# Kernel optimization log

Hardware: AMD Instinct MI355X
Metric: run time of the kernel (lower is better)

Reference implementation:

```python
import jax, jax.numpy as jnp
import numpy as np

DIM = 2048; KV_RANK = 512; Q_RANK = 768; H = 16
D_NR = 128; D_R = 64; D_V = 128
B = 8; L = 32; MAX_T = 4096; START = MAX_T - L
QK_DIM = D_NR + D_R
SCALE = 1.0 / float(np.sqrt(QK_DIM))
EPS = 1.1920929e-07  # torch.finfo(float32).eps (nn.RMSNorm default)
ROPE_BASE = 10000.0


def rms_norm(x, w):
    return x * jax.lax.rsqrt(jnp.mean(x * x, axis=-1, keepdims=True) + EPS) * w


def apply_rope(x, cos, sin):
    # x: (b, l, h, d) with d even; cos/sin: (l, d//2) -> complex multiply on pairs
    b, l, h, d = x.shape
    xp = x.reshape(b, l, h, d // 2, 2)
    xr, xi = xp[..., 0], xp[..., 1]
    c = cos[None, :, None, :]
    s = sin[None, :, None, :]
    return jnp.stack([xr * c - xi * s, xr * s + xi * c], axis=-1).reshape(b, l, h, d)


def setup_inputs() -> dict:
    key = jax.random.key(0)
    ks = jax.random.split(key, 9)
    w = 0.02
    # rotary angles for absolute positions START..START+L-1
    inv_freq = 1.0 / (ROPE_BASE ** (np.arange(0, D_R, 2, dtype=np.float32) / D_R))  # (32,)
    pos = np.arange(START, START + L, dtype=np.float32)
    ang = pos[:, None] * inv_freq[None, :]  # (L, 32)
    # causal mask over full cache: query i sits at absolute position START+i
    t = jnp.arange(MAX_T)[None, :]
    qpos = START + jnp.arange(L)[:, None]
    mask = jnp.where(t <= qpos, 0.0, -1e30).astype(jnp.float32)  # (L, MAX_T)
    return {
        "x": jax.random.normal(ks[0], (B, L, DIM), dtype=jnp.float32),
        "start_pos": START,
        "freq_cos": jnp.asarray(np.cos(ang), dtype=jnp.float32),
        "freq_sin": jnp.asarray(np.sin(ang), dtype=jnp.float32),
        "mask": mask,
        "kv_latent_cache": jax.random.normal(ks[1], (B, MAX_T, KV_RANK), dtype=jnp.float32) * 0.05,
        "k_rope_cache": jax.random.normal(ks[2], (B, MAX_T, D_R), dtype=jnp.float32) * 0.05,
        "w_kv_down": jax.random.normal(ks[3], (KV_RANK + D_R, DIM), dtype=jnp.float32) * w,
        "w_q_down": jax.random.normal(ks[4], (Q_RANK, DIM), dtype=jnp.float32) * w,
        "rms_q_w": jnp.ones((Q_RANK,), dtype=jnp.float32),
        "w_q_up": jax.random.normal(ks[5], (H * QK_DIM, Q_RANK), dtype=jnp.float32) * w,
        "w_kv_up": jax.random.normal(ks[6], (H * (D_NR + D_V), KV_RANK), dtype=jnp.float32) * w,
        "w_out": jax.random.normal(ks[7], (DIM, H * D_V), dtype=jnp.float32) * w,
    }


def reference(x, start_pos, freq_cos, freq_sin, mask, kv_latent_cache, k_rope_cache,
              w_kv_down, w_q_down, rms_q_w, w_q_up, w_kv_up, w_out):
    b, l, _ = x.shape
    end_pos = start_pos + l
    # query path: down-proj -> RMSNorm -> up-proj (NOTE: module's rms_norm_kv is unused)
    q = rms_norm(x @ w_q_down.T, rms_q_w) @ w_q_up.T
    q = q.reshape(b, l, H, QK_DIM)
    q_nrope, q_rope = q[..., :D_NR], q[..., D_NR:]
    q_rope = apply_rope(q_rope, freq_cos, freq_sin)
    # latent kv path
    kv = x @ w_kv_down.T  # (b, l, KV_RANK + D_R)
    kv_latent, k_rope = kv[..., :KV_RANK], kv[..., KV_RANK:]
    k_rope = apply_rope(k_rope[:, :, None, :], freq_cos, freq_sin)[:, :, 0, :]
    # scatter-write into caches, then read prefix [:end_pos]
    kvc = kv_latent_cache.at[:, start_pos:end_pos].set(kv_latent)[:, :end_pos]  # (b, t, k)
    krc = k_rope_cache.at[:, start_pos:end_pos].set(k_rope)[:, :end_pos]        # (b, t, r)
    # weight absorption
    w_up = w_kv_up.reshape(H, D_NR + D_V, KV_RANK)
    q_abs = jnp.einsum('blhd,hdk->blhk', q_nrope, w_up[:, :D_NR])
    scores = (jnp.einsum('blhk,btk->blht', q_abs, kvc)
              + jnp.einsum('blhr,btr->blht', q_rope, krc)) * SCALE
    scores = scores + mask[None, :, None, :]
    p = jax.nn.softmax(scores, axis=-1)
    o = jnp.einsum('blht,btk->blhk', p, kvc)
    o = jnp.einsum('blhk,hdk->blhd', o, w_up[:, D_NR:])
    return o.reshape(b, l, H * D_V) @ w_out.T
```

## Files before the change

### kernel.cpp

```cpp
#include <hip/hip_runtime.h>
#include <math.h>

#define DIMX 2048
#define KV_RANK 512
#define Q_RANK 768
#define NH 16
#define D_NR 128
#define D_R 64
#define D_V 128
#define NB 8
#define NL 32
#define MAX_T 4096
#define STARTP (MAX_T - NL)
#define QK_DIM (D_NR + D_R)
#define ATT_SCALE 0.07216878364870323f
#define RMS_EPS 1.1920929e-07f

typedef unsigned short u16;
typedef __attribute__((ext_vector_type(4))) unsigned short u16x4;
typedef __attribute__((ext_vector_type(8))) unsigned short u16x8;
typedef __attribute__((ext_vector_type(8))) short short8;
typedef __attribute__((ext_vector_type(4))) float f32x4;

#define GLOBAL_AS __attribute__((address_space(1)))
#define LDS_AS __attribute__((address_space(3)))

#define NDOWN 1344
#define DPART ((long long)256 * NDOWN)

__device__ inline u16 f2b(float f) {
    union { float f; unsigned u; } v; v.f = f;
    unsigned r = (v.u + 0x7fffu + ((v.u >> 16) & 1u)) >> 16;
    return (u16)r;
}
__device__ inline float b2f(u16 u) {
    union { unsigned u; float f; } v; v.u = ((unsigned)u) << 16; return v.f;
}

template<int BM, int BN, int OUTMODE, bool GSWZ, bool DEEP>
__global__ __launch_bounds__(256) void gemm_mfma(
    const u16* __restrict__ A, const u16* __restrict__ B, void* __restrict__ Cv,
    float* __restrict__ rs,
    int K, int lda, int ldb, int ldc,
    long long sA1, long long sA2, long long sB1, long long sB2,
    long long sC1, long long sC2, int nb2)
{
    constexpr int MFR = BM / 32;
    constexpr int NFR = BN / 32;
    constexpr int nA = BM / 16;
    constexpr int nB = BN / 16;
    constexpr int NBUF = DEEP ? 3 : 2;
    static_assert(!DEEP || (nA % 4 == 0 && nB % 4 == 0), "DEEP needs uniform loads/wave");

    int bx = blockIdx.x, by = blockIdx.y, bz = blockIdx.z;
    if (GSWZ) {
        int flat = bx + gridDim.x * (by + gridDim.y * bz);
        int nwg = gridDim.x * gridDim.y * gridDim.z;
        int lf = (flat & 7) * (nwg >> 3) + (flat >> 3);
        bx = lf % gridDim.x;
        int r = lf / gridDim.x;
        by = r % gridDim.y;
        bz = r / gridDim.y;
    }
    const int z1 = bz / nb2, z2 = bz % nb2;
    A += z1 * sA1 + z2 * sA2;
    B += z1 * sB1 + z2 * sB2;

    const int m0 = by * BM;
    const int n0 = bx * BN;
    const int tid = threadIdx.x;
    const int lane = tid & 63;
    const int wid = tid >> 6;
    const int wm = wid >> 1, wn = wid & 1;
    const int l15 = lane & 15;
    const int l4  = lane >> 4;

    __shared__ __align__(16) u16 As[NBUF][BM * 32];
    __shared__ __align__(16) u16 Bs[NBUF][BN * 32];

    auto stage = [&](int buf, int k0) {
        #pragma unroll
        for (int j = 0; j < nA / 4 + 1; ++j) {
            int jj = wid + j * 4;
            if (jj < nA) {
                int c = jj * 64 + lane;
                int row = c >> 2;
                int ksg = (c & 3) ^ ((row >> 1) & 3);
                const u16* src = A + (long long)(m0 + row) * lda + k0 + ksg * 8;
                __builtin_amdgcn_global_load_lds((const GLOBAL_AS void*)src,
                                                 (LDS_AS void*)&As[buf][jj * 512], 16, 0, 0);
            }
        }
        #pragma unroll
        for (int j = 0; j < nB / 4 + 1; ++j) {
            int jj = wid + j * 4;
            if (jj < nB) {
                int c = jj * 64 + lane;
                int row = c >> 2;
                int ksg = (c & 3) ^ ((row >> 1) & 3);
                const u16* src = B + (long long)(n0 + row) * ldb + k0 + ksg * 8;
                __builtin_amdgcn_global_load_lds((const GLOBAL_AS void*)src,
                                                 (LDS_AS void*)&Bs[buf][jj * 512], 16, 0, 0);
            }
        }
    };

    f32x4 acc[MFR][NFR];
    #pragma unroll
    for (int i = 0; i < MFR; ++i)
        #pragma unroll
        for (int j = 0; j < NFR; ++j)
            acc[i][j] = (f32x4)0.0f;

    const int nk = K >> 5;

    if (DEEP) {
        constexpr int LPW = nA / 4 + nB / 4;
        stage(0, 0);
        if (nk > 1) stage(1, 32);
        for (int ki = 0; ki < nk; ++ki) {
            const int r = ki % 3;
            if (ki + 1 < nk)
                asm volatile("s_waitcnt vmcnt(%0)" :: "i"(LPW) : "memory");
            else
                asm volatile("s_waitcnt vmcnt(0)" ::: "memory");
            __builtin_amdgcn_s_barrier();
            __builtin_amdgcn_sched_barrier(0);

            short8 a[MFR], b[NFR];
            #pragma unroll
            for (int mf = 0; mf < MFR; ++mf) {
                int row = wm * 16 * MFR + mf * 16 + l15;
                int ksl = l4 ^ ((row >> 1) & 3);
                a[mf] = *(const short8*)&As[r][row * 32 + ksl * 8];
            }
            #pragma unroll
            for (int nf = 0; nf < NFR; ++nf) {
                int row = wn * 16 * NFR + nf * 16 + l15;
                int ksl = l4 ^ ((row >> 1) & 3);
                b[nf] = *(const short8*)&Bs[r][row * 32 + ksl * 8];
            }
            if (ki + 2 < nk) stage((ki + 2) % 3, (ki + 2) << 5);

            __builtin_amdgcn_s_setprio(1);
            #pragma unroll
            for (int mf = 0; mf < MFR; ++mf)
                #pragma unroll
                for (int nf = 0; nf < NFR; ++nf)
                    acc[mf][nf] = __builtin_amdgcn_mfma_f32_16x16x32_bf16(
                        a[mf], b[nf], acc[mf][nf], 0, 0, 0);
            __builtin_amdgcn_s_setprio(0);
        }
    } else {
        stage(0, 0);
        int cur = 0;
        for (int ki = 0; ki < nk; ++ki) {
            __syncthreads();
            if (ki + 1 < nk) stage(cur ^ 1, (ki + 1) << 5);

            short8 a[MFR], b[NFR];
            #pragma unroll
            for (int mf = 0; mf < MFR; ++mf) {
                int row = wm * 16 * MFR + mf * 16 + l15;
                int ksl = l4 ^ ((row >> 1) & 3);
                a[mf] = *(const short8*)&As[cur][row * 32 + ksl * 8];
            }
            #pragma unroll
            for (int nf = 0; nf < NFR; ++nf) {
                int row = wn * 16 * NFR + nf * 16 + l15;
                int ksl = l4 ^ ((row >> 1) & 3);
                b[nf] = *(const short8*)&Bs[cur][row * 32 + ksl * 8];
            }
            __builtin_amdgcn_s_setprio(1);
            #pragma unroll
            for (int mf = 0; mf < MFR; ++mf)
                #pragma unroll
                for (int nf = 0; nf < NFR; ++nf)
                    acc[mf][nf] = __builtin_amdgcn_mfma_f32_16x16x32_bf16(
                        a[mf], b[nf], acc[mf][nf], 0, 0, 0);
            __builtin_amdgcn_s_setprio(0);
            cur ^= 1;
        }
    }

    if (OUTMODE == 2) {
        u16* C = (u16*)Cv + z1 * sC1 + z2 * sC2;
        float rowp[MFR][4];
        #pragma unroll
        for (int mf = 0; mf < MFR; ++mf)
            #pragma unroll
            for (int r = 0; r < 4; ++r)
                rowp[mf][r] = 0.f;
        #pragma unroll
        for (int mf = 0; mf < MFR; ++mf) {
            #pragma unroll
            for (int nf = 0; nf < NFR; ++nf) {
                int r0 = m0 + wm * 16 * MFR + mf * 16 + l4 * 4;
                int c0 = n0 + wn * 16 * NFR + nf * 16 + l15;
                #pragma unroll
                for (int r = 0; r < 4; ++r) {
                    int row = r0 + r;
                    int vlen = STARTP + (row & 31) + 1;
                    float p = (c0 < vlen) ? __expf(acc[mf][nf][r] * ATT_SCALE) : 0.f;
                    u16 pb = f2b(p);
                    C[(long long)row * ldc + c0] = pb;
                    rowp[mf][r] += b2f(pb);
                }
            }
        }
        #pragma unroll
        for (int mf = 0; mf < MFR; ++mf)
            #pragma unroll
            for (int r = 0; r < 4; ++r) {
                float v = rowp[mf][r];
                v += __shfl_xor(v, 1);
                v += __shfl_xor(v, 2);
                v += __shfl_xor(v, 4);
                v += __shfl_xor(v, 8);
                if (l15 == 0) {
                    int row = m0 + wm * 16 * MFR + mf * 16 + l4 * 4 + r;
                    atomicAdd(&rs[z1 * 512 + row], v);
                }
            }
    } else if (OUTMODE == 1) {
        u16* C = (u16*)Cv + z1 * sC1 + z2 * sC2;
        #pragma unroll
        for (int mf = 0; mf < MFR; ++mf)
            #pragma unroll
            for (int nf = 0; nf < NFR; ++nf) {
                int r0 = m0 + wm * 16 * MFR + mf * 16 + l4 * 4;
                int c0 = n0 + wn * 16 * NFR + nf * 16 + l15;
                #pragma unroll
                for (int r = 0; r < 4; ++r)
                    C[(long long)(r0 + r) * ldc + c0] = f2b(acc[mf][nf][r]);
            }
    } else {
        float* C = (float*)Cv + z1 * sC1 + z2 * sC2;
        #pragma unroll
        for (int mf = 0; mf < MFR; ++mf)
            #pragma unroll
            for (int nf = 0; nf < NFR; ++nf) {
                int r0 = m0 + wm * 16 * MFR + mf * 16 + l4 * 4;
                int c0 = n0 + wn * 16 * NFR + nf * 16 + l15;
                #pragma unroll
                for (int r = 0; r < 4; ++r)
                    C[(long long)(r0 + r) * ldc + c0] = acc[mf][nf][r];
            }
    }
}

struct Segs {
    const float* src[6];
    u16* dst[6];
    int n4[6];
};
__global__ __launch_bounds__(256) void f2b_multi(Segs s)
{
    int seg = blockIdx.y;
    int i = blockIdx.x * 256 + threadIdx.x;
    if (i >= s.n4[seg]) return;
    float4 v = ((const float4*)s.src[seg])[i];
    u16x4 o = { f2b(v.x), f2b(v.y), f2b(v.z), f2b(v.w) };
    ((u16x4*)s.dst[seg])[i] = o;
}

__global__ __launch_bounds__(256) void rs_zero(float* __restrict__ rs)
{
    int i = blockIdx.x * 256 + threadIdx.x;
    float4 z = { 0.f, 0.f, 0.f, 0.f };
    ((float4*)rs)[i] = z;
}

__global__ __launch_bounds__(256) void rms_reduce(const float* __restrict__ part,
                                                  const float* __restrict__ w,
                                                  u16* __restrict__ outb)
{
    const int row = blockIdx.x;
    const int tid = threadIdx.x;
    __shared__ float red[256];
    float val[3];
    float s = 0.f;
    #pragma unroll
    for (int j = 0; j < 3; ++j) {
        int i = tid + j * 256;
        long long off = (long long)row * NDOWN + i;
        float v = part[off] + part[DPART + off] + part[2 * DPART + off] + part[3 * DPART + off];
        val[j] = v;
        s += v * v;
    }
    red[tid] = s; __syncthreads();
    for (int off = 128; off > 0; off >>= 1) {
        if (tid < off) red[tid] += red[tid + off];
        __syncthreads();
    }
    float scale = rsqrtf(red[0] / (float)Q_RANK + RMS_EPS);
    u16* ob = outb + (long long)row * Q_RANK;
    #pragma unroll
    for (int j = 0; j < 3; ++j) {
        int i = tid + j * 256;
        ob[i] = f2b(val[j] * scale * w[i]);
    }
}

__global__ __launch_bounds__(256) void wuT_kernel(const float* __restrict__ w,
                                                  u16* __restrict__ outp)
{
    __shared__ u16 T[64][65];
    const int h = blockIdx.z;
    const int y0 = blockIdx.y * 64;
    const int x0 = blockIdx.x * 64;
    const int tid = threadIdx.x;
    #pragma unroll
    for (int i = 0; i < 16; ++i) {
        int lin = i * 256 + tid;
        int r = lin >> 6, c = lin & 63;
        T[c][r] = f2b(w[((long long)h * 256 + y0 + r) * 512 + x0 + c]);
    }
    __syncthreads();
    #pragma unroll
    for (int i = 0; i < 16; ++i) {
        int lin = i * 256 + tid;
        int r = lin >> 6, c = lin & 63;
        outp[((long long)h * 512 + x0 + r) * 128 + y0 + c] = T[r][c];
    }
}

__global__ __launch_bounds__(256) void bcat_new_reduce(const float* __restrict__ part,
                                                       const float* __restrict__ fc,
                                                       const float* __restrict__ fs,
                                                       u16* __restrict__ bcat)
{
    const int bl = blockIdx.x;
    const int b = bl >> 5, l = bl & 31;
    const int t = threadIdx.x;
    if (t >= 144) return;
    long long off = (long long)bl * NDOWN + 768 + 4 * t;
    float4 v0 = *(const float4*)(part + off);
    float4 v1 = *(const float4*)(part + DPART + off);
    float4 v2 = *(const float4*)(part + 2 * DPART + off);
    float4 v3 = *(const float4*)(part + 3 * DPART + off);
    float4 v = { v0.x + v1.x + v2.x + v3.x, v0.y + v1.y + v2.y + v3.y,
                 v0.z + v1.z + v2.z + v3.z, v0.w + v1.w + v2.w + v3.w };
    u16* dst = bcat + ((long long)b * MAX_T + STARTP + l) * 576;
    if (t < 128) {
        u16x4 o = { f2b(v.x), f2b(v.y), f2b(v.z), f2b(v.w) };
        ((u16x4*)dst)[t] = o;
    } else {
        int g = t - 128;
        float c0 = fc[l * 32 + 2 * g],     s0 = fs[l * 32 + 2 * g];
        float c1 = fc[l * 32 + 2 * g + 1], s1 = fs[l * 32 + 2 * g + 1];
        u16x4 o = { f2b(v.x * c0 - v.y * s0), f2b(v.x * s0 + v.y * c0),
                    f2b(v.z * c1 - v.w * s1), f2b(v.z * s1 + v.w * c1) };
        *(u16x4*)(dst + 512 + 4 * g) = o;
    }
}

__global__ __launch_bounds__(256) void prep_cache(const float* __restrict__ kvc,
                                                  const float* __restrict__ krc,
                                                  u16* __restrict__ bcat,
                                                  u16* __restrict__ kvcT)
{
    const int b = blockIdx.z;
    const int t0 = blockIdx.y * 64;
    const int tid = threadIdx.x;

    if (blockIdx.x == 8) {
        #pragma unroll
        for (int i = 0; i < 2; ++i) {
            int lin = i * 256 + tid;
            int r = lin >> 3, c8 = lin & 7;
            int t = t0 + r;
            if (t >= STARTP) continue;
            const float* src = krc + ((long long)b * MAX_T + t) * D_R + 8 * c8;
            float4 v0 = *(const float4*)src;
            float4 v1 = *(const float4*)(src + 4);
            u16x8 o = { f2b(v0.x), f2b(v0.y), f2b(v0.z), f2b(v0.w),
                        f2b(v1.x), f2b(v1.y), f2b(v1.z), f2b(v1.w) };
            *(u16x8*)(bcat + ((long long)b * MAX_T + t) * 576 + 512 + 8 * c8) = o;
        }
        return;
    }

    __shared__ u16 T[64 * 64];
    const int k0 = blockIdx.x * 64;

    #pragma unroll
    for (int i = 0; i < 2; ++i) {
        int lin = i * 256 + tid;
        int r = lin >> 3, c8 = lin & 7;
        int t = t0 + r;
        u16x4 oa, ob;
        if (t < STARTP) {
            const float* src = kvc + ((long long)b * MAX_T + t) * KV_RANK + k0 + 8 * c8;
            float4 v0 = *(const float4*)src;
            float4 v1 = *(const float4*)(src + 4);
            oa[0] = f2b(v0.x); oa[1] = f2b(v0.y); oa[2] = f2b(v0.z); oa[3] = f2b(v0.w);
            ob[0] = f2b(v1.x); ob[1] = f2b(v1.y); ob[2] = f2b(v1.z); ob[3] = f2b(v1.w);
            u16x8 o = { oa[0], oa[1], oa[2], oa[3], ob[0], ob[1], ob[2], ob[3] };
            *(u16x8*)(bcat + ((long long)b * MAX_T + t) * 576 + k0 + 8 * c8) = o;
        } else {
            const u16* s = bcat + ((long long)b * MAX_T + t) * 576 + k0 + 8 * c8;
            oa = *(const u16x4*)s;
            ob = *(const u16x4*)(s + 4);
        }
        int tg = r >> 2, te = r & 3;
        int c4a = 2 * c8, c4b = 2 * c8 + 1;
        int cola = ((tg ^ c4a) << 2) + te;
        int colb = ((tg ^ c4b) << 2) + te;
        #pragma unroll
        for (int j = 0; j < 4; ++j) {
            T[(4 * c4a + j) * 64 + cola] = oa[j];
            T[(4 * c4b + j) * 64 + colb] = ob[j];
        }
    }
    __syncthreads();

    u16* outp = kvcT + ((long long)b * KV_RANK + k0) * MAX_T + t0;
    #pragma unroll
    for (int i = 0; i < 2; ++i) {
        int lin = i * 256 + tid;
        int k = lin >> 3, c8 = lin & 7;
        int s = k >> 2;
        u16x4 va = *(const u16x4*)&T[k * 64 + (((2 * c8) ^ s) << 2)];
        u16x4 vb = *(const u16x4*)&T[k * 64 + (((2 * c8 + 1) ^ s) << 2)];
        u16x8 o = { va[0], va[1], va[2], va[3], vb[0], vb[1], vb[2], vb[3] };
        *(u16x8*)(outp + (long long)k * MAX_T + 8 * c8) = o;
    }
}

__global__ __launch_bounds__(256) void rope_q(const u16* __restrict__ qb,
                                              const float* __restrict__ fc,
                                              const float* __restrict__ fs,
                                              u16* __restrict__ qprimeb)
{
    int idx = blockIdx.x * 256 + threadIdx.x;
    int i = idx & 31;
    int h = (idx >> 5) & (NH - 1);
    int l = (idx >> 9) & (NL - 1);
    int b = idx >> 14;
    const u16* src = qb + (long long)(b * NL + l) * 3072 + h * QK_DIM + D_NR + 2 * i;
    float xr = b2f(src[0]), xi = b2f(src[1]);
    float c = fc[l * 32 + i], s = fs[l * 32 + i];
    u16* dst = qprimeb + ((long long)(b * NH + h) * NL + l) * 576 + 512 + 2 * i;
    dst[0] = f2b(xr * c - xi * s);
    dst[1] = f2b(xr * s + xi * c);
}

__global__ __launch_bounds__(256) void reduce_pv(const float* __restrict__ part,
                                                 const float* __restrict__ rs,
                                                 u16* __restrict__ o_hb)
{
    int idx = blockIdx.x * 256 + threadIdx.x;
    int b = idx >> 16;
    int i4 = idx & 65535;
    int m = i4 >> 7;
    const float* p = part + (long long)b * 1048576 + 4 * i4;
    float4 v0 = *(const float4*)p;
    float4 v1 = *(const float4*)(p + 262144);
    float4 v2 = *(const float4*)(p + 524288);
    float4 v3 = *(const float4*)(p + 786432);
    float inv = 1.0f / rs[b * 512 + m];
    u16x4 o = { f2b((v0.x + v1.x + v2.x + v3.x) * inv),
                f2b((v0.y + v1.y + v2.y + v3.y) * inv),
                f2b((v0.z + v1.z + v2.z + v3.z) * inv),
                f2b((v0.w + v1.w + v2.w + v3.w) * inv) };
    ((u16x4*)(o_hb + (long long)b * 262144))[i4] = o;
}

__global__ __launch_bounds__(256) void reduce_out(const float* __restrict__ part,
                                                  float* __restrict__ out)
{
    int idx = blockIdx.x * 256 + threadIdx.x;
    const float* p = part + 4 * (long long)idx;
    float4 v0 = *(const float4*)p;
    float4 v1 = *(const float4*)(p + 524288);
    float4 v2 = *(const float4*)(p + 1048576);
    float4 v3 = *(const float4*)(p + 1572864);
    float4 o = { v0.x + v1.x + v2.x + v3.x, v0.y + v1.y + v2.y + v3.y,
                 v0.z + v1.z + v2.z + v3.z, v0.w + v1.w + v2.w + v3.w };
    ((float4*)out)[idx] = o;
}

extern "C" void kernel_launch(void* const* d_in, const int* in_sizes, int n_in,
                              void* d_out, int out_size, void* d_ws, size_t ws_size,
                              hipStream_t stream)
{
    const float* x        = (const float*)d_in[0];
    const float* fc       = (const float*)d_in[2];
    const float* fs       = (const float*)d_in[3];
    const float* kvc      = (const float*)d_in[5];
    const float* krc      = (const float*)d_in[6];
    const float* w_kv_down= (const float*)d_in[7];
    const float* w_q_down = (const float*)d_in[8];
    const float* rms_q_w  = (const float*)d_in[9];
    const float* w_q_up   = (const float*)d_in[10];
    const float* w_kv_up  = (const float*)d_in[11];
    const float* w_out    = (const float*)d_in[12];
    float* out            = (float*)d_out;

    float* down_part = (float*)d_ws;
    float* rs      = down_part + 1376256;
    u16* pb        = (u16*)(rs + 4096);
    u16* base      = pb + 16777216;
    u16* xb      = base;                 base += 524288;
    u16* qdb     = base;                 base += 196608;
    u16* qb      = base;                 base += 786432;
    u16* qprimeb = base;                 base += 2359296;
    u16* wqkv_b  = base;                 base += 2752512;
    u16* wqu_b   = base;                 base += 2359296;
    u16* wkvu_b  = base;                 base += 2097152;
    u16* wout_b  = base;                 base += 4194304;
    u16* wuT     = base;                 base += 1048576;
    u16* bcat    = base;                 base += 18874368;
    u16* kvcT    = base;                 base += 16777216;
    u16* o_hb    = base;                 base += 2097152;
    u16* o_upb   = base;                 base += 524288;
    float* pv_part  = (float*)bcat;
    float* out_part = (float*)kvcT;

    Segs segs;
    segs.src[0] = x;         segs.dst[0] = xb;                  segs.n4[0] = 131072;
    segs.src[1] = w_q_down;  segs.dst[1] = wqkv_b;              segs.n4[1] = 393216;
    segs.src[2] = w_q_up;    segs.dst[2] = wqu_b;               segs.n4[2] = 589824;
    segs.src[3] = w_kv_down; segs.dst[3] = wqkv_b + 768 * 2048; segs.n4[3] = 294912;
    segs.src[4] = w_kv_up;   segs.dst[4] = wkvu_b;              segs.n4[4] = 524288;
    segs.src[5] = w_out;     segs.dst[5] = wout_b;              segs.n4[5] = 1048576;
    f2b_multi<<<dim3(4096, 6), 256, 0, stream>>>(segs);

    rs_zero<<<4, 256, 0, stream>>>(rs);
    wuT_kernel<<<dim3(8, 2, 16), 256, 0, stream>>>(w_kv_up, wuT);

    gemm_mfma<32, 64, 0, true, false><<<dim3(21, 8, 4), 256, 0, stream>>>(
        xb, wqkv_b, down_part, nullptr, 512, 2048, 2048, NDOWN,
        0LL, 512LL, 0LL, 512LL, 0LL, DPART, 4);
    rms_reduce<<<256, 256, 0, stream>>>(down_part, rms_q_w, qdb);
    gemm_mfma<32, 64, 1, true, false><<<dim3(48, 8, 1), 256, 0, stream>>>(
        qdb, wqu_b, qb, nullptr, 768, 768, 768, 3072, 0, 0, 0, 0, 0, 0, 1);
    bcat_new_reduce<<<256, 256, 0, stream>>>(down_part, fc, fs, bcat);
    prep_cache<<<dim3(9, 64, 8), 256, 0, stream>>>(kvc, krc, bcat, kvcT);

    gemm_mfma<32, 128, 1, true, false><<<dim3(4, 1, 128), 256, 0, stream>>>(
        qb, wuT, qprimeb, nullptr, 128, 3072, 128, 576,
        98304LL, 192LL, 0LL, 65536LL, 294912LL, 18432LL, 16);
    rope_q<<<512, 256, 0, stream>>>(qb, fc, fs, qprimeb);

    gemm_mfma<128, 128, 2, true, true><<<dim3(32, 4, 8), 256, 0, stream>>>(
        qprimeb, bcat, pb, rs, 576, 576, 576, 4096,
        294912LL, 0LL, 2359296LL, 0LL, 2097152LL, 0LL, 1);
    gemm_mfma<128, 128, 0, true, true><<<dim3(4, 4, 32), 256, 0, stream>>>(
        pb, kvcT, pv_part, nullptr, 1024, 4096, 4096, 512,
        2097152LL, 1024LL, 2097152LL, 1024LL, 1048576LL, 262144LL, 4);
    reduce_pv<<<2048, 256, 0, stream>>>(pv_part, rs, o_hb);

    gemm_mfma<32, 64, 1, true, false><<<dim3(2, 1, 128), 256, 0, stream>>>(
        o_hb, wkvu_b + 128 * 512, o_upb, nullptr, 512, 512, 512, 2048,
        262144LL, 16384LL, 0LL, 131072LL, 65536LL, 128LL, 16);
    gemm_mfma<32, 64, 0, true, false><<<dim3(32, 8, 4), 256, 0, stream>>>(
        o_upb, wout_b, out_part, nullptr, 512, 2048, 2048, 2048,
        0LL, 512LL, 0LL, 512LL, 0LL, 524288LL, 4);
    reduce_out<<<512, 256, 0, stream>>>(out_part, out);
}
```

Baseline: 314.8 us.

## Split cache prep into bcat build and transpose, shrink attention GEMM tiles

Replaces the fused prep_cache kernel with two kernels. bcat_build converts the fp32 latent and rope caches to bf16 in one fully coalesced pass and is launched early, before the down-projection GEMM. kvcT_build then transposes from the bf16 bcat buffer using larger 64x256 shared tiles with an XOR swizzle. The scores and PV GEMMs also move from 128x128 to 64x128 tiles, doubling grid size for better CU occupancy. The cost is an extra read of bcat and an extra kernel launch.

```diff
diff --git a/kernel.cpp b/kernel.cpp
--- a/kernel.cpp
+++ b/kernel.cpp
@@ -355,76 +355,55 @@
     }
 }
 
-__global__ __launch_bounds__(256) void prep_cache(const float* __restrict__ kvc,
+__global__ __launch_bounds__(256) void bcat_build(const float* __restrict__ kvc,
                                                   const float* __restrict__ krc,
-                                                  u16* __restrict__ bcat,
+                                                  u16* __restrict__ bcat)
+{
+    const int b = blockIdx.y;
+    const int t0 = blockIdx.x * 32;
+    const int tid = threadIdx.x;
+    #pragma unroll
+    for (int i = 0; i < 9; ++i) {
+        int lin = i * 256 + tid;
+        int r = lin / 72, c8 = lin % 72;
+        int t = t0 + r;
+        const float* src = (c8 < 64)
+            ? kvc + ((long long)b * MAX_T + t) * KV_RANK + 8 * c8
+            : krc + ((long long)b * MAX_T + t) * D_R + 8 * (c8 - 64);
+        float4 v0 = *(const float4*)src;
+        float4 v1 = *(const float4*)(src + 4);
+        u16x8 o = { f2b(v0.x), f2b(v0.y), f2b(v0.z), f2b(v0.w),
+                    f2b(v1.x), f2b(v1.y), f2b(v1.z), f2b(v1.w) };
+        *(u16x8*)(bcat + ((long long)b * MAX_T + t) * 576 + 8 * c8) = o;
+    }
+}
+
+__global__ __launch_bounds__(256) void kvcT_build(const u16* __restrict__ bcat,
                                                   u16* __restrict__ kvcT)
 {
+    __shared__ u16 T[64 * 256];
     const int b = blockIdx.z;
-    const int t0 = blockIdx.y * 64;
+    const int t0 = blockIdx.y * 256;
+    const int k0 = blockIdx.x * 64;
     const int tid = threadIdx.x;
-
-    if (blockIdx.x == 8) {
-        #pragma unroll
-        for (int i = 0; i < 2; ++i) {
-            int lin = i * 256 + tid;
-            int r = lin >> 3, c8 = lin & 7;
-            int t = t0 + r;
-            if (t >= STARTP) continue;
-            const float* src = krc + ((long long)b * MAX_T + t) * D_R + 8 * c8;
-            float4 v0 = *(const float4*)src;
-            float4 v1 = *(const float4*)(src + 4);
-            u16x8 o = { f2b(v0.x), f2b(v0.y), f2b(v0.z), f2b(v0.w),
-                        f2b(v1.x), f2b(v1.y), f2b(v1.z), f2b(v1.w) };
-            *(u16x8*)(bcat + ((long long)b * MAX_T + t) * 576 + 512 + 8 * c8) = o;
-        }
-        return;
-    }
-
-    __shared__ u16 T[64 * 64];
-    const int k0 = blockIdx.x * 64;
-
-    #pragma unroll
-    for (int i = 0; i < 2; ++i) {
+    #pragma unroll
+    for (int i = 0; i < 8; ++i) {
         int lin = i * 256 + tid;
-        int r = lin >> 3, c8 = lin & 7;
-        int t = t0 + r;
-        u16x4 oa, ob;
-        if (t < STARTP) {
-            const float* src = kvc + ((long long)b * MAX_T + t) * KV_RANK + k0 + 8 * c8;
-            float4 v0 = *(const float4*)src;
-            float4 v1 = *(const float4*)(src + 4);
-            oa[0] = f2b(v0.x); oa[1] = f2b(v0.y); oa[2] = f2b(v0.z); oa[3] = f2b(v0.w);
-            ob[0] = f2b(v1.x); ob[1] = f2b(v1.y); ob[2] = f2b(v1.z); ob[3] = f2b(v1.w);
-            u16x8 o = { oa[0], oa[1], oa[2], oa[3], ob[0], ob[1], ob[2], ob[3] };
-            *(u16x8*)(bcat + ((long long)b * MAX_T + t) * 576 + k0 + 8 * c8) = o;
-        } else {
-            const u16* s = bcat + ((long long)b * MAX_T + t) * 576 + k0 + 8 * c8;
-            oa = *(const u16x4*)s;
-            ob = *(const u16x4*)(s + 4);
-        }
-        int tg = r >> 2, te = r & 3;
-        int c4a = 2 * c8, c4b = 2 * c8 + 1;
-        int cola = ((tg ^ c4a) << 2) + te;
-        int colb = ((tg ^ c4b) << 2) + te;
-        #pragma unroll
-        for (int j = 0; j < 4; ++j) {
-            T[(4 * c4a + j) * 64 + cola] = oa[j];
-            T[(4 * c4b + j) * 64 + colb] = ob[j];
-        }
+        int t = lin >> 3, c8 = lin & 7;
+        u16x8 v = *(const u16x8*)(bcat + ((long long)b * MAX_T + t0 + t) * 576 + k0 + 8 * c8);
+        int colo = (t >> 3) ^ c8;
+        #pragma unroll
+        for (int j = 0; j < 8; ++j)
+            T[(8 * c8 + j) * 256 + (colo << 3) + (t & 7)] = v[j];
     }
     __syncthreads();
-
     u16* outp = kvcT + ((long long)b * KV_RANK + k0) * MAX_T + t0;
     #pragma unroll
-    for (int i = 0; i < 2; ++i) {
+    for (int i = 0; i < 8; ++i) {
         int lin = i * 256 + tid;
-        int k = lin >> 3, c8 = lin & 7;
-        int s = k >> 2;
-        u16x4 va = *(const u16x4*)&T[k * 64 + (((2 * c8) ^ s) << 2)];
-        u16x4 vb = *(const u16x4*)&T[k * 64 + (((2 * c8 + 1) ^ s) << 2)];
-        u16x8 o = { va[0], va[1], va[2], va[3], vb[0], vb[1], vb[2], vb[3] };
-        *(u16x8*)(outp + (long long)k * MAX_T + 8 * c8) = o;
+        int k = lin >> 5, t8 = lin & 31;
+        u16x8 v = *(const u16x8*)&T[k * 256 + ((t8 ^ (k >> 3)) << 3)];
+        *(u16x8*)(outp + (long long)k * MAX_T + 8 * t8) = v;
     }
 }
 
@@ -529,6 +508,7 @@
 
     rs_zero<<<4, 256, 0, stream>>>(rs);
     wuT_kernel<<<dim3(8, 2, 16), 256, 0, stream>>>(w_kv_up, wuT);
+    bcat_build<<<dim3(127, 8), 256, 0, stream>>>(kvc, krc, bcat);
 
     gemm_mfma<32, 64, 0, true, false><<<dim3(21, 8, 4), 256, 0, stream>>>(
         xb, wqkv_b, down_part, nullptr, 512, 2048, 2048, NDOWN,
@@ -537,17 +517,17 @@
     gemm_mfma<32, 64, 1, true, false><<<dim3(48, 8, 1), 256, 0, stream>>>(
         qdb, wqu_b, qb, nullptr, 768, 768, 768, 3072, 0, 0, 0, 0, 0, 0, 1);
     bcat_new_reduce<<<256, 256, 0, stream>>>(down_part, fc, fs, bcat);
-    prep_cache<<<dim3(9, 64, 8), 256, 0, stream>>>(kvc, krc, bcat, kvcT);
+    kvcT_build<<<dim3(8, 16, 8), 256, 0, stream>>>(bcat, kvcT);
 
     gemm_mfma<32, 128, 1, true, false><<<dim3(4, 1, 128), 256, 0, stream>>>(
         qb, wuT, qprimeb, nullptr, 128, 3072, 128, 576,
         98304LL, 192LL, 0LL, 65536LL, 294912LL, 18432LL, 16);
     rope_q<<<512, 256, 0, stream>>>(qb, fc, fs, qprimeb);
 
-    gemm_mfma<128, 128, 2, true, true><<<dim3(32, 4, 8), 256, 0, stream>>>(
+    gemm_mfma<64, 128, 2, true, true><<<dim3(32, 8, 8), 256, 0, stream>>>(
         qprimeb, bcat, pb, rs, 576, 576, 576, 4096,
         294912LL, 0LL, 2359296LL, 0LL, 2097152LL, 0LL, 1);
-    gemm_mfma<128, 128, 0, true, true><<<dim3(4, 4, 32), 256, 0, stream>>>(
+    gemm_mfma<64, 128, 0, true, true><<<dim3(4, 8, 32), 256, 0, stream>>>(
         pb, kvcT, pv_part, nullptr, 1024, 4096, 4096, 512,
         2097152LL, 1024LL, 2097152LL, 1024LL, 1048576LL, 262144LL, 4);
     reduce_pv<<<2048, 256, 0, stream>>>(pv_part, rs, o_hb);
```

After: 329.3 us. 4.6% more time.
